# Performance work log

Hardware: AMD Instinct MI355X
Metric: run time of the kernel (lower is better)

Reference implementation:

```python
import jax, jax.numpy as jnp
import numpy as np
import math

B, H, S, D = 2, 16, 2048, 128
INV_SCALE = math.sqrt(D)  # divisor applied to QK^T logits (dropout_p = 0.0)


def setup_inputs() -> dict:
    key = jax.random.key(0)
    kq, kk, kv = jax.random.split(key, 3)
    return {
        "query": jax.random.normal(kq, (B, H, S, D), dtype=jnp.float32),
        "key": jax.random.normal(kk, (B, H, S, D), dtype=jnp.float32),
        "value": jax.random.normal(kv, (B, H, S, D), dtype=jnp.float32),
    }


def reference(query, key, value):
    # v1 = Q @ K^T ; v2 = v1 / inv_scale ; v3 = softmax(v2, -1) ; dropout(p=0) is identity ; out = v3 @ V
    scores = jnp.einsum("bhqd,bhkd->bhqk", query, key) / INV_SCALE  # [B,H,Sq,Sk]
    probs = jax.nn.softmax(scores, axis=-1)
    return jnp.einsum("bhqk,bhkd->bhqd", probs, value)  # [B,H,Sq,D]
```

## Files before the change

kernel.cpp:

```cpp
#include <hip/hip_runtime.h>
#include <hip/hip_bf16.h>

typedef __bf16 bf16x8 __attribute__((ext_vector_type(8)));
typedef float f32x4 __attribute__((ext_vector_type(4)));

#define S_LEN 2048
#define D_DIM 128
#define BH 32
#define BN 64
#define NT (S_LEN / BN)
#define NWAVE 8
#define QSCALE (0.08838834764831845f * 1.4426950408889634f)


__global__ __launch_bounds__(512, 2)
void fa_fwd_kernel(const float* __restrict__ Qg, const float* __restrict__ Kg,
                   const float* __restrict__ Vg, float* __restrict__ Og) {
    __shared__ __bf16 Klds[2][BN][D_DIM + 8];
    __shared__ __bf16 Vlds[2][D_DIM][BN + 8];
    __shared__ __bf16 Plds[NWAVE][32][BN + 8];

    const int bh   = blockIdx.x & (BH - 1);
    const int qt   = blockIdx.x >> 5;
    const int tid  = threadIdx.x;
    const int wave = tid >> 6;
    const int lane = tid & 63;
    const int quad = lane >> 4;
    const int m16  = lane & 15;

    const float* Qh = Qg + bh * (S_LEN * D_DIM);
    const float* Kh = Kg + bh * (S_LEN * D_DIM);
    const float* Vh = Vg + bh * (S_LEN * D_DIM);
    float*       Oh = Og + bh * (S_LEN * D_DIM);

    const int qrow_base = qt * 256 + wave * 32;

    bf16x8 qf[2][4];
#pragma unroll
    for (int mf = 0; mf < 2; ++mf)
#pragma unroll
        for (int ks = 0; ks < 4; ++ks) {
            const float* qp = Qh + (qrow_base + mf * 16 + m16) * D_DIM + ks * 32 + quad * 8;
            const float4 a = *(const float4*)(qp);
            const float4 b = *(const float4*)(qp + 4);
            bf16x8 f;
            f[0] = (__bf16)(a.x * QSCALE); f[1] = (__bf16)(a.y * QSCALE);
            f[2] = (__bf16)(a.z * QSCALE); f[3] = (__bf16)(a.w * QSCALE);
            f[4] = (__bf16)(b.x * QSCALE); f[5] = (__bf16)(b.y * QSCALE);
            f[6] = (__bf16)(b.z * QSCALE); f[7] = (__bf16)(b.w * QSCALE);
            qf[mf][ks] = f;
        }

    f32x4 o_acc[2][8];
#pragma unroll
    for (int mf = 0; mf < 2; ++mf)
#pragma unroll
        for (int nt = 0; nt < 8; ++nt) {
            o_acc[mf][nt][0] = 0.f; o_acc[mf][nt][1] = 0.f;
            o_acc[mf][nt][2] = 0.f; o_acc[mf][nt][3] = 0.f;
        }
    float l_part[2][4] = {{0.f, 0.f, 0.f, 0.f}, {0.f, 0.f, 0.f, 0.f}};

    const int krow = tid >> 3;
    const int kc   = (tid & 7) * 16;
    const int vd0   = (tid & 63) * 2;
    const int vgrp  = tid >> 6;
    const int vslot = (vgrp ^ ((vd0 >> 3) & 7)) << 3;

    float4 kreg[4];
    float2 vreg[8];
    {
        const float* kg = Kh + krow * D_DIM + kc;
        kreg[0] = *(const float4*)(kg);
        kreg[1] = *(const float4*)(kg + 4);
        kreg[2] = *(const float4*)(kg + 8);
        kreg[3] = *(const float4*)(kg + 12);
        const float* vp = Vh + vgrp * 8 * D_DIM + vd0;
#pragma unroll
        for (int kr = 0; kr < 8; ++kr)
            vreg[kr] = *(const float2*)(vp + kr * D_DIM);
    }
    {
        bf16x8 w;
        w[0] = (__bf16)kreg[0].x; w[1] = (__bf16)kreg[0].y;
        w[2] = (__bf16)kreg[0].z; w[3] = (__bf16)kreg[0].w;
        w[4] = (__bf16)kreg[1].x; w[5] = (__bf16)kreg[1].y;
        w[6] = (__bf16)kreg[1].z; w[7] = (__bf16)kreg[1].w;
        *(bf16x8*)&Klds[0][krow][kc] = w;
        w[0] = (__bf16)kreg[2].x; w[1] = (__bf16)kreg[2].y;
        w[2] = (__bf16)kreg[2].z; w[3] = (__bf16)kreg[2].w;
        w[4] = (__bf16)kreg[3].x; w[5] = (__bf16)kreg[3].y;
        w[6] = (__bf16)kreg[3].z; w[7] = (__bf16)kreg[3].w;
        *(bf16x8*)&Klds[0][krow][kc + 8] = w;
        bf16x8 w0, w1;
#pragma unroll
        for (int kr = 0; kr < 8; ++kr) {
            w0[kr] = (__bf16)vreg[kr].x;
            w1[kr] = (__bf16)vreg[kr].y;
        }
        *(bf16x8*)&Vlds[0][vd0][vslot]     = w0;
        *(bf16x8*)&Vlds[0][vd0 + 1][vslot] = w1;
    }
    __syncthreads();

    for (int kt = 0; kt < NT; ++kt) {
        const int cur = kt & 1;

        if (kt + 1 < NT) {
            const float* kg = Kh + (kt + 1) * (BN * D_DIM) + krow * D_DIM + kc;
            kreg[0] = *(const float4*)(kg);
            kreg[1] = *(const float4*)(kg + 4);
            kreg[2] = *(const float4*)(kg + 8);
            kreg[3] = *(const float4*)(kg + 12);
            const float* vp = Vh + (kt + 1) * (BN * D_DIM) + vgrp * 8 * D_DIM + vd0;
#pragma unroll
            for (int kr = 0; kr < 8; ++kr)
                vreg[kr] = *(const float2*)(vp + kr * D_DIM);
        }

        f32x4 sacc[2][4];
#pragma unroll
        for (int mf = 0; mf < 2; ++mf)
#pragma unroll
            for (int nt = 0; nt < 4; ++nt) {
                sacc[mf][nt][0] = 0.f; sacc[mf][nt][1] = 0.f;
                sacc[mf][nt][2] = 0.f; sacc[mf][nt][3] = 0.f;
            }
        __builtin_amdgcn_s_setprio(1);
#pragma unroll
        for (int ks = 0; ks < 4; ++ks)
#pragma unroll
            for (int nt = 0; nt < 4; ++nt) {
                const bf16x8 kf = *(const bf16x8*)&Klds[cur][nt * 16 + m16][ks * 32 + quad * 8];
                sacc[0][nt] = __builtin_amdgcn_mfma_f32_16x16x32_bf16(qf[0][ks], kf, sacc[0][nt], 0, 0, 0);
                sacc[1][nt] = __builtin_amdgcn_mfma_f32_16x16x32_bf16(qf[1][ks], kf, sacc[1][nt], 0, 0, 0);
            }
        __builtin_amdgcn_s_setprio(0);

#pragma unroll
        for (int mf = 0; mf < 2; ++mf)
#pragma unroll
            for (int nt = 0; nt < 4; ++nt)
#pragma unroll
                for (int r = 0; r < 4; ++r) {
                    const float p = __builtin_amdgcn_exp2f(sacc[mf][nt][r]);
                    l_part[mf][r] += p;
                    Plds[wave][mf * 16 + quad * 4 + r][nt * 16 + m16] = (__bf16)p;
                }

        if (kt + 1 < NT) {
            const int nxt = cur ^ 1;
            bf16x8 w;
            w[0] = (__bf16)kreg[0].x; w[1] = (__bf16)kreg[0].y;
            w[2] = (__bf16)kreg[0].z; w[3] = (__bf16)kreg[0].w;
            w[4] = (__bf16)kreg[1].x; w[5] = (__bf16)kreg[1].y;
            w[6] = (__bf16)kreg[1].z; w[7] = (__bf16)kreg[1].w;
            *(bf16x8*)&Klds[nxt][krow][kc] = w;
            w[0] = (__bf16)kreg[2].x; w[1] = (__bf16)kreg[2].y;
            w[2] = (__bf16)kreg[2].z; w[3] = (__bf16)kreg[2].w;
            w[4] = (__bf16)kreg[3].x; w[5] = (__bf16)kreg[3].y;
            w[6] = (__bf16)kreg[3].z; w[7] = (__bf16)kreg[3].w;
            *(bf16x8*)&Klds[nxt][krow][kc + 8] = w;
            bf16x8 w0, w1;
#pragma unroll
            for (int kr = 0; kr < 8; ++kr) {
                w0[kr] = (__bf16)vreg[kr].x;
                w1[kr] = (__bf16)vreg[kr].y;
            }
            *(bf16x8*)&Vlds[nxt][vd0][vslot]     = w0;
            *(bf16x8*)&Vlds[nxt][vd0 + 1][vslot] = w1;
        }

        __builtin_amdgcn_s_setprio(1);
#pragma unroll
        for (int ks = 0; ks < 2; ++ks) {
            const bf16x8 pa0 = *(const bf16x8*)&Plds[wave][m16]     [ks * 32 + quad * 8];
            const bf16x8 pa1 = *(const bf16x8*)&Plds[wave][16 + m16][ks * 32 + quad * 8];
#pragma unroll
            for (int nt = 0; nt < 8; ++nt) {
                const int d = nt * 16 + m16;
                const bf16x8 vf =
                    *(const bf16x8*)&Vlds[cur][d][((ks * 4 + quad) ^ ((d >> 3) & 7)) << 3];
                o_acc[0][nt] = __builtin_amdgcn_mfma_f32_16x16x32_bf16(pa0, vf, o_acc[0][nt], 0, 0, 0);
                o_acc[1][nt] = __builtin_amdgcn_mfma_f32_16x16x32_bf16(pa1, vf, o_acc[1][nt], 0, 0, 0);
            }
        }
        __builtin_amdgcn_s_setprio(0);

        __syncthreads();
    }

#pragma unroll
    for (int xm = 1; xm <= 8; xm <<= 1)
#pragma unroll
        for (int mf = 0; mf < 2; ++mf)
#pragma unroll
            for (int r = 0; r < 4; ++r)
                l_part[mf][r] += __shfl_xor(l_part[mf][r], xm, 64);

#pragma unroll
    for (int mf = 0; mf < 2; ++mf) {
        float inv[4];
#pragma unroll
        for (int r = 0; r < 4; ++r) inv[r] = 1.0f / l_part[mf][r];
#pragma unroll
        for (int nt = 0; nt < 8; ++nt)
#pragma unroll
            for (int r = 0; r < 4; ++r)
                Oh[(qrow_base + mf * 16 + quad * 4 + r) * D_DIM + nt * 16 + m16] =
                    o_acc[mf][nt][r] * inv[r];
    }
}

extern "C" void kernel_launch(void* const* d_in, const int* in_sizes, int n_in,
                              void* d_out, int out_size, void* d_ws, size_t ws_size,
                              hipStream_t stream) {
    const float* Q = (const float*)d_in[0];
    const float* K = (const float*)d_in[1];
    const float* V = (const float*)d_in[2];
    float* O = (float*)d_out;
    dim3 grid(BH * (S_LEN / 256));
    fa_fwd_kernel<<<grid, 512, 0, stream>>>(Q, K, V, O);
}
```

Baseline: 201.7 us.

## Compute S transposed to keep P in registers, drop P LDS round-trip

The QK^T MFMA operands are swapped so each lane holds scores for one query row across key columns. That register layout lets the bf16 probabilities feed the PV MFMA directly as the A operand, removing the per-wave P staging buffer in LDS and its write/read traffic. The V tile is stored with a permuted column order so key indices match the new P register layout. Row sums now reduce across quads and are redistributed with shuffles, which adds a little epilogue complexity.

New measurement: 196.8 us. 2.4% less time.

```diff
diff --git a/kernel.cpp b/kernel.cpp
--- a/kernel.cpp
+++ b/kernel.cpp
@@ -2,6 +2,7 @@
 #include <hip/hip_bf16.h>
 
 typedef __bf16 bf16x8 __attribute__((ext_vector_type(8)));
+typedef __bf16 bf16x4 __attribute__((ext_vector_type(4)));
 typedef float f32x4 __attribute__((ext_vector_type(4)));
 
 #define S_LEN 2048
@@ -18,7 +19,6 @@
                    const float* __restrict__ Vg, float* __restrict__ Og) {
     __shared__ __bf16 Klds[2][BN][D_DIM + 8];
     __shared__ __bf16 Vlds[2][D_DIM][BN + 8];
-    __shared__ __bf16 Plds[NWAVE][32][BN + 8];
 
     const int bh   = blockIdx.x & (BH - 1);
     const int qt   = blockIdx.x >> 5;
@@ -59,13 +59,17 @@
             o_acc[mf][nt][0] = 0.f; o_acc[mf][nt][1] = 0.f;
             o_acc[mf][nt][2] = 0.f; o_acc[mf][nt][3] = 0.f;
         }
-    float l_part[2][4] = {{0.f, 0.f, 0.f, 0.f}, {0.f, 0.f, 0.f, 0.f}};
+    float l_part[2] = {0.f, 0.f};
 
     const int krow = tid >> 3;
     const int kc   = (tid & 7) * 16;
     const int vd0   = (tid & 63) * 2;
     const int vgrp  = tid >> 6;
-    const int vslot = (vgrp ^ ((vd0 >> 3) & 7)) << 3;
+    const int vswz  = (vd0 >> 3) & 7;
+    const int slotA = (4 * (vgrp >> 2) + 2 * (vgrp & 1));
+    const int offA  = 4 * ((vgrp >> 1) & 1);
+    const int colA  = ((slotA ^ vswz) << 3) + offA;
+    const int colB  = (((slotA + 1) ^ vswz) << 3) + offA;
 
     float4 kreg[4];
     float2 vreg[8];
@@ -92,14 +96,16 @@
         w[4] = (__bf16)kreg[3].x; w[5] = (__bf16)kreg[3].y;
         w[6] = (__bf16)kreg[3].z; w[7] = (__bf16)kreg[3].w;
         *(bf16x8*)&Klds[0][krow][kc + 8] = w;
-        bf16x8 w0, w1;
-#pragma unroll
-        for (int kr = 0; kr < 8; ++kr) {
-            w0[kr] = (__bf16)vreg[kr].x;
-            w1[kr] = (__bf16)vreg[kr].y;
-        }
-        *(bf16x8*)&Vlds[0][vd0][vslot]     = w0;
-        *(bf16x8*)&Vlds[0][vd0 + 1][vslot] = w1;
+        bf16x4 a0, b0, a1, b1;
+#pragma unroll
+        for (int j = 0; j < 4; ++j) {
+            a0[j] = (__bf16)vreg[j].x;     b0[j] = (__bf16)vreg[4 + j].x;
+            a1[j] = (__bf16)vreg[j].y;     b1[j] = (__bf16)vreg[4 + j].y;
+        }
+        *(bf16x4*)&Vlds[0][vd0][colA]     = a0;
+        *(bf16x4*)&Vlds[0][vd0][colB]     = b0;
+        *(bf16x4*)&Vlds[0][vd0 + 1][colA] = a1;
+        *(bf16x4*)&Vlds[0][vd0 + 1][colB] = b1;
     }
     __syncthreads();
 
@@ -132,11 +138,12 @@
 #pragma unroll
             for (int nt = 0; nt < 4; ++nt) {
                 const bf16x8 kf = *(const bf16x8*)&Klds[cur][nt * 16 + m16][ks * 32 + quad * 8];
-                sacc[0][nt] = __builtin_amdgcn_mfma_f32_16x16x32_bf16(qf[0][ks], kf, sacc[0][nt], 0, 0, 0);
-                sacc[1][nt] = __builtin_amdgcn_mfma_f32_16x16x32_bf16(qf[1][ks], kf, sacc[1][nt], 0, 0, 0);
+                sacc[0][nt] = __builtin_amdgcn_mfma_f32_16x16x32_bf16(kf, qf[0][ks], sacc[0][nt], 0, 0, 0);
+                sacc[1][nt] = __builtin_amdgcn_mfma_f32_16x16x32_bf16(kf, qf[1][ks], sacc[1][nt], 0, 0, 0);
             }
         __builtin_amdgcn_s_setprio(0);
 
+        bf16x8 pa[2][2];
 #pragma unroll
         for (int mf = 0; mf < 2; ++mf)
 #pragma unroll
@@ -144,8 +151,8 @@
 #pragma unroll
                 for (int r = 0; r < 4; ++r) {
                     const float p = __builtin_amdgcn_exp2f(sacc[mf][nt][r]);
-                    l_part[mf][r] += p;
-                    Plds[wave][mf * 16 + quad * 4 + r][nt * 16 + m16] = (__bf16)p;
+                    l_part[mf] += p;
+                    pa[mf][nt >> 1][(nt & 1) * 4 + r] = (__bf16)p;
                 }
 
         if (kt + 1 < NT) {
@@ -161,28 +168,28 @@
             w[4] = (__bf16)kreg[3].x; w[5] = (__bf16)kreg[3].y;
             w[6] = (__bf16)kreg[3].z; w[7] = (__bf16)kreg[3].w;
             *(bf16x8*)&Klds[nxt][krow][kc + 8] = w;
-            bf16x8 w0, w1;
-#pragma unroll
-            for (int kr = 0; kr < 8; ++kr) {
-                w0[kr] = (__bf16)vreg[kr].x;
-                w1[kr] = (__bf16)vreg[kr].y;
-            }
-            *(bf16x8*)&Vlds[nxt][vd0][vslot]     = w0;
-            *(bf16x8*)&Vlds[nxt][vd0 + 1][vslot] = w1;
+            bf16x4 a0, b0, a1, b1;
+#pragma unroll
+            for (int j = 0; j < 4; ++j) {
+                a0[j] = (__bf16)vreg[j].x;     b0[j] = (__bf16)vreg[4 + j].x;
+                a1[j] = (__bf16)vreg[j].y;     b1[j] = (__bf16)vreg[4 + j].y;
+            }
+            *(bf16x4*)&Vlds[nxt][vd0][colA]     = a0;
+            *(bf16x4*)&Vlds[nxt][vd0][colB]     = b0;
+            *(bf16x4*)&Vlds[nxt][vd0 + 1][colA] = a1;
+            *(bf16x4*)&Vlds[nxt][vd0 + 1][colB] = b1;
         }
 
         __builtin_amdgcn_s_setprio(1);
 #pragma unroll
         for (int ks = 0; ks < 2; ++ks) {
-            const bf16x8 pa0 = *(const bf16x8*)&Plds[wave][m16]     [ks * 32 + quad * 8];
-            const bf16x8 pa1 = *(const bf16x8*)&Plds[wave][16 + m16][ks * 32 + quad * 8];
 #pragma unroll
             for (int nt = 0; nt < 8; ++nt) {
                 const int d = nt * 16 + m16;
                 const bf16x8 vf =
                     *(const bf16x8*)&Vlds[cur][d][((ks * 4 + quad) ^ ((d >> 3) & 7)) << 3];
-                o_acc[0][nt] = __builtin_amdgcn_mfma_f32_16x16x32_bf16(pa0, vf, o_acc[0][nt], 0, 0, 0);
-                o_acc[1][nt] = __builtin_amdgcn_mfma_f32_16x16x32_bf16(pa1, vf, o_acc[1][nt], 0, 0, 0);
+                o_acc[0][nt] = __builtin_amdgcn_mfma_f32_16x16x32_bf16(pa[0][ks], vf, o_acc[0][nt], 0, 0, 0);
+                o_acc[1][nt] = __builtin_amdgcn_mfma_f32_16x16x32_bf16(pa[1][ks], vf, o_acc[1][nt], 0, 0, 0);
             }
         }
         __builtin_amdgcn_s_setprio(0);
@@ -191,18 +198,17 @@
     }
 
 #pragma unroll
-    for (int xm = 1; xm <= 8; xm <<= 1)
-#pragma unroll
-        for (int mf = 0; mf < 2; ++mf)
-#pragma unroll
-            for (int r = 0; r < 4; ++r)
-                l_part[mf][r] += __shfl_xor(l_part[mf][r], xm, 64);
-
-#pragma unroll
     for (int mf = 0; mf < 2; ++mf) {
+        l_part[mf] += __shfl_xor(l_part[mf], 16, 64);
+        l_part[mf] += __shfl_xor(l_part[mf], 32, 64);
+    }
+
+#pragma unroll
+    for (int mf = 0; mf < 2; ++mf) {
+        const float inv_own = 1.0f / l_part[mf];
         float inv[4];
 #pragma unroll
-        for (int r = 0; r < 4; ++r) inv[r] = 1.0f / l_part[mf][r];
+        for (int r = 0; r < 4; ++r) inv[r] = __shfl(inv_own, quad * 4 + r, 64);
 #pragma unroll
         for (int nt = 0; nt < 8; ++nt)
 #pragma unroll
```
